# Performance work log

Hardware: AMD Instinct MI355X
Metric: run time of the kernel (lower is better)

The kernel has to match this reference:

```python
import jax, jax.numpy as jnp
import numpy as np

D_NODE, C, N_HEAD = 256, 32, 8
N_SEQ, N_RES = 256, 256
LN_EPS = 1e-5
MASK_BIAS = 1e9


def setup_inputs() -> dict:
    key = jax.random.key(0)
    ks = jax.random.split(key, 4)
    return {
        "M_raw": jax.random.normal(ks[0], (N_SEQ, N_RES, D_NODE), dtype=jnp.float32),
        "M_mask": jnp.ones((N_SEQ, N_RES), dtype=jnp.float32),
        "ln_w": jnp.ones((D_NODE,), jnp.float32),
        "ln_b": jnp.zeros((D_NODE,), jnp.float32),
        "qkv_w": jax.random.normal(ks[1], (D_NODE, 3 * N_HEAD * C), jnp.float32) * (D_NODE ** -0.5),
        "gate_w": jax.random.normal(ks[2], (D_NODE, N_HEAD * C), jnp.float32) * (D_NODE ** -0.5),
        "gate_b": jnp.ones((N_HEAD * C,), jnp.float32),
        "out_w": jax.random.normal(ks[3], (N_HEAD * C, D_NODE), jnp.float32) * ((N_HEAD * C) ** -0.5),
        "out_b": jnp.zeros((D_NODE,), jnp.float32),
    }


def reference(M_raw, M_mask, ln_w, ln_b, qkv_w, gate_w, gate_b, out_w, out_b):
    # Transpose to column-attention layout: [N_res, N_seq, d]
    M = jnp.swapaxes(M_raw, -2, -3)
    mask = jnp.swapaxes(M_mask, -1, -2)  # [N_res, N_seq]

    # LayerNorm over feature dim
    mu = jnp.mean(M, axis=-1, keepdims=True)
    var = jnp.mean(jnp.square(M - mu), axis=-1, keepdims=True)
    Mn = (M - mu) * jax.lax.rsqrt(var + LN_EPS) * ln_w + ln_b

    # QKV projection (no bias), split heads
    r, s = Mn.shape[0], Mn.shape[1]
    qkv = (Mn @ qkv_w).reshape(r, s, 3, N_HEAD, C)
    q, k, v = qkv[:, :, 0], qkv[:, :, 1], qkv[:, :, 2]  # [r, s, h, c]
    q = q * (C ** -0.5)

    # Masked attention over the sequence (column) axis
    logits = jnp.einsum('rqhc,rkhc->rhqk', q, k)
    logits = logits + (MASK_BIAS * (mask - 1.0))[:, None, None, :]
    weights = jax.nn.softmax(logits, axis=-1)
    o = jnp.einsum('rhqk,rkhc->rqhc', weights, v).reshape(r, s, N_HEAD * C)

    # Sigmoid gating and output projection
    gate = jax.nn.sigmoid(Mn @ gate_w + gate_b)
    out = (o * gate) @ out_w + out_b

    # Residual in original layout
    return M_raw + jnp.swapaxes(out, -2, -3)
```

## Files before the change

### kernel.cpp

```cpp
#include <hip/hip_runtime.h>


typedef short bf16x8 __attribute__((ext_vector_type(8)));
typedef float f32x4  __attribute__((ext_vector_type(4)));
typedef float f32x16 __attribute__((ext_vector_type(16)));

union U8 { uint w[4]; bf16x8 v; ushort u[8]; };

__device__ __forceinline__ ushort f2bf(float f) {
  uint u = __float_as_uint(f);
  u = (u + 0x7fffu + ((u >> 16) & 1u)) >> 16;
  return (ushort)u;
}

__device__ __forceinline__ uint pk2(float lo, float hi) {
  return (uint)f2bf(lo) | ((uint)f2bf(hi) << 16);
}

__device__ __forceinline__ f32x16 MFMA32(bf16x8 a, bf16x8 b, f32x16 c) {
  return __builtin_amdgcn_mfma_f32_32x32x16_bf16(a, b, c, 0, 0, 0);
}
__device__ __forceinline__ f32x4 MFMA16(bf16x8 a, bf16x8 b, f32x4 c) {
  return __builtin_amdgcn_mfma_f32_16x16x32_bf16(a, b, c, 0, 0, 0);
}

__device__ __forceinline__ bf16x8 ldG8(const ushort* __restrict__ p, int row, int ko) {
  return *(const bf16x8*)(p + (size_t)row * 256 + ko);
}

__device__ __forceinline__ f32x16 zero16() {
  f32x16 z;
  #pragma unroll
  for (int i = 0; i < 16; ++i) z[i] = 0.f;
  return z;
}

__global__ __launch_bounds__(256) void k_prep(const float* __restrict__ qkv_w,
                                              const float* __restrict__ gate_w,
                                              const float* __restrict__ out_w,
                                              ushort* __restrict__ ws) {
  __shared__ ushort t[64][72];
  const int b = blockIdx.x;
  const float* src; ushort* dst; int C, r0, c0; bool scale_q = false;
  if (b < 48)      { src = qkv_w;  dst = ws;          C = 768; r0 = (b/12)*64;      c0 = (b%12)*64; scale_q = true; }
  else if (b < 64) { int bb = b-48; src = gate_w; dst = ws + 196608; C = 256; r0 = (bb>>2)*64; c0 = (bb&3)*64; }
  else             { int bb = b-64; src = out_w;  dst = ws + 262144; C = 256; r0 = (bb>>2)*64; c0 = (bb&3)*64; }
  const int tid = threadIdx.x;
  const int cc = tid & 63, rb = tid >> 6;
  #pragma unroll
  for (int j = 0; j < 16; ++j) {
    const int rr = j*4 + rb;
    float v = src[(size_t)(r0+rr)*C + c0 + cc];
    if (scale_q && (c0+cc) < 256) v *= 0.17677669529663687f;
    t[cc][rr] = f2bf(v);
  }
  __syncthreads();
  const int dd = (tid & 31)*2, cb = tid >> 5;
  #pragma unroll
  for (int j = 0; j < 8; ++j) {
    const int c2 = j*8 + cb;
    const uint wv = (uint)t[c2][dd] | ((uint)t[c2][dd+1] << 16);
    *(uint*)(dst + (size_t)(c0+c2)*256 + r0 + dd) = wv;
  }
}

#define KOFF 0
#define VOFF 20480
#define GOFF 37376

__global__ __launch_bounds__(512, 2) void k_attn(
    const float* __restrict__ M_raw, const float* __restrict__ M_mask,
    const float* __restrict__ ln_w, const float* __restrict__ ln_b,
    const ushort* __restrict__ qkv_wT, const ushort* __restrict__ gate_wT,
    const float* __restrict__ gate_b, ushort* __restrict__ og)
{
  extern __shared__ char smem[];
  const int r    = blockIdx.x;
  const int tid  = threadIdx.x;
  const int w    = tid >> 6;
  const int lane = tid & 63;
  const int l31  = lane & 31;
  const int hl   = lane >> 5;
  const int Q0   = w << 5;
  const int s    = Q0 + l31;

  const float* rowp = M_raw + (size_t)s * 65536 + (size_t)r * 256;
  float4 xa[16], xb[16];
  float sum = 0.f, sq = 0.f;
  #pragma unroll
  for (int dt = 0; dt < 16; ++dt) {
    xa[dt] = *(const float4*)(rowp + dt*16 + hl*8);
    xb[dt] = *(const float4*)(rowp + dt*16 + hl*8 + 4);
    sum += xa[dt].x + xa[dt].y + xa[dt].z + xa[dt].w
         + xb[dt].x + xb[dt].y + xb[dt].z + xb[dt].w;
    sq  += xa[dt].x*xa[dt].x + xa[dt].y*xa[dt].y + xa[dt].z*xa[dt].z + xa[dt].w*xa[dt].w
         + xb[dt].x*xb[dt].x + xb[dt].y*xb[dt].y + xb[dt].z*xb[dt].z + xb[dt].w*xb[dt].w;
  }
  sum += __shfl_xor(sum, 32, 64);
  sq  += __shfl_xor(sq,  32, 64);
  const float mu = sum * 0.00390625f;
  const float rs = rsqrtf(sq * 0.00390625f - mu*mu + 1e-5f);
  bf16x8 mn[16];
  #pragma unroll
  for (int dt = 0; dt < 16; ++dt) {
    const float4 wa = *(const float4*)(ln_w + dt*16 + hl*8);
    const float4 wb = *(const float4*)(ln_w + dt*16 + hl*8 + 4);
    const float4 ba = *(const float4*)(ln_b + dt*16 + hl*8);
    const float4 bb = *(const float4*)(ln_b + dt*16 + hl*8 + 4);
    U8 u;
    u.w[0] = pk2((xa[dt].x-mu)*rs*wa.x+ba.x, (xa[dt].y-mu)*rs*wa.y+ba.y);
    u.w[1] = pk2((xa[dt].z-mu)*rs*wa.z+ba.z, (xa[dt].w-mu)*rs*wa.w+ba.w);
    u.w[2] = pk2((xb[dt].x-mu)*rs*wb.x+bb.x, (xb[dt].y-mu)*rs*wb.y+bb.y);
    u.w[3] = pk2((xb[dt].z-mu)*rs*wb.z+bb.z, (xb[dt].w-mu)*rs*wb.w+bb.w);
    mn[dt] = u.v;
  }

  uint m0=0, m1=0, m2=0, m3=0;
  for (int b = 0; b < 32; ++b) {
    const int k0 = ((b>>4)<<5) + (b&3) + (((b>>2)&3)<<3) + hl*4;
    m0 |= (M_mask[(size_t)(k0      )*256 + r] > 0.5f ? 1u:0u) << b;
    m1 |= (M_mask[(size_t)(k0 +  64)*256 + r] > 0.5f ? 1u:0u) << b;
    m2 |= (M_mask[(size_t)(k0 + 128)*256 + r] > 0.5f ? 1u:0u) << b;
    m3 |= (M_mask[(size_t)(k0 + 192)*256 + r] > 0.5f ? 1u:0u) << b;
  }
  const bool full = ((m0 & m1 & m2 & m3) == 0xFFFFFFFFu);

  auto mergeOp = [&](float q0, float q1, float q2, float q3,
                     float q4, float q5, float q6, float q7) -> bf16x8 {
    const uint x0 = pk2(q0, q1), x1 = pk2(q2, q3);
    const uint z0 = pk2(q4, q5), z1 = pk2(q6, q7);
    const uint xx0 = __shfl_xor(x0, 32, 64), xx1 = __shfl_xor(x1, 32, 64);
    const uint zz0 = __shfl_xor(z0, 32, 64), zz1 = __shfl_xor(z1, 32, 64);
    U8 u;
    u.w[0] = hl ? zz0 : x0;
    u.w[1] = hl ? zz1 : x1;
    u.w[2] = hl ? z0  : xx0;
    u.w[3] = hl ? z1  : xx1;
    return u.v;
  };

  auto projT = [&](const ushort* __restrict__ W, int rowbase) -> f32x16 {
    f32x16 acc = zero16();
    #pragma unroll
    for (int dt = 0; dt < 16; ++dt)
      acc = MFMA32(ldG8(W, rowbase + l31, dt*16 + hl*8), mn[dt], acc);
    return acc;
  };
  auto projN = [&](const ushort* __restrict__ W, int rowbase) -> f32x16 {
    f32x16 acc = zero16();
    #pragma unroll
    for (int dt = 0; dt < 16; ++dt)
      acc = MFMA32(mn[dt], ldG8(W, rowbase + l31, dt*16 + hl*8), acc);
    return acc;
  };
  auto packB = [&](const f32x16& q, bf16x8& lo, bf16x8& hi2) {
    lo  = mergeOp(q[0], q[1], q[2],  q[3],  q[4],  q[5],  q[6],  q[7]);
    hi2 = mergeOp(q[8], q[9], q[10], q[11], q[12], q[13], q[14], q[15]);
  };
  auto stageKV = [&](const f32x16& KA, const f32x16& VA) {
    #pragma unroll
    for (int rq = 0; rq < 4; ++rq) {
      uint2 p2;
      p2.x = pk2(KA[4*rq],   KA[4*rq+1]);
      p2.y = pk2(KA[4*rq+2], KA[4*rq+3]);
      *(uint2*)(smem + KOFF + s*80 + rq*16 + hl*8) = p2;
      p2.x = pk2(VA[4*rq],   VA[4*rq+1]);
      p2.y = pk2(VA[4*rq+2], VA[4*rq+3]);
      *(uint2*)(smem + VOFF + l31*528 + Q0*2 + rq*16 + hl*8) = p2;
    }
  };

  bf16x8 bq0, bq1;
  {
    f32x16 KA = projT(qkv_wT, 256 + 0);
    f32x16 VA = projN(qkv_wT, 512 + 0);
    stageKV(KA, VA);
    f32x16 QA = projT(qkv_wT, 0);
    packB(QA, bq0, bq1);
  }
  __syncthreads();

  for (int hd = 0; hd < 8; ++hd) {
    const int hs = hd << 5;

    float m_ = -3.0e38f, l_ = 0.f;
    f32x16 O = zero16();
    #pragma unroll
    for (int kt = 0; kt < 8; ++kt) {
      const bf16x8 a0 = *(const bf16x8*)(smem + KOFF + (kt*32 + l31)*80 + hl*16);
      const bf16x8 a1 = *(const bf16x8*)(smem + KOFF + (kt*32 + l31)*80 + 32 + hl*16);
      f32x16 S = MFMA32(a0, bq0, zero16());
      S = MFMA32(a1, bq1, S);

      float pmax = S[0];
      #pragma unroll
      for (int i = 1; i < 16; ++i) pmax = fmaxf(pmax, S[i]);
      pmax = fmaxf(pmax, __shfl_xor(pmax, 32, 64));

      if (!__all(pmax <= m_ + 8.0f)) {
        const float mnew = fmaxf(m_, pmax);
        const float sc = __expf(m_ - mnew);
        #pragma unroll
        for (int i = 0; i < 16; ++i) O[i] *= sc;
        l_ *= sc;
        m_ = mnew;
      }

      #pragma unroll
      for (int i = 0; i < 16; ++i) {
        float p = __expf(S[i] - m_);
        if (!full) {
          const int bi = kt*16 + i;
          const uint mw = (bi < 32) ? m0 : (bi < 64) ? m1 : (bi < 96) ? m2 : m3;
          p = ((mw >> (bi & 31)) & 1u) ? p : 0.f;
        }
        S[i] = p; l_ += p;
      }

      const bf16x8 pa0 = mergeOp(S[0], S[1], S[2],  S[3],  S[4],  S[5],  S[6],  S[7]);
      const bf16x8 vb0 = *(const bf16x8*)(smem + VOFF + l31*528 + kt*64 + hl*16);
      O = MFMA32(vb0, pa0, O);
      const bf16x8 pa1 = mergeOp(S[8], S[9], S[10], S[11], S[12], S[13], S[14], S[15]);
      const bf16x8 vb1 = *(const bf16x8*)(smem + VOFF + l31*528 + kt*64 + 32 + hl*16);
      O = MFMA32(vb1, pa1, O);
    }
    l_ += __shfl_xor(l_, 32, 64);
    const float inv = 1.0f / l_;

    f32x16 G = projT(gate_wT, hs);
    const int sxor = (s >> 1) & 15;
    #pragma unroll
    for (int ep = 0; ep < 8; ++ep) {
      const int e0 = 2*ep;
      const int c0 = (e0 & 3) + 8*(e0 >> 2) + 4*hl;
      const float g0 = gate_b[hs + c0];
      const float g1 = gate_b[hs + c0 + 1];
      const float v0 = O[e0]   * inv / (1.f + __expf(-(G[e0]   + g0)));
      const float v1 = O[e0+1] * inv / (1.f + __expf(-(G[e0+1] + g1)));
      const int cpair = (ep & 1) + 4*(ep >> 1) + 2*hl;
      *(uint*)(smem + GOFF + s*64 + ((cpair ^ sxor) << 2)) = pk2(v0, v1);
    }

    __syncthreads();

    uint* ogw = (uint*)og;
    const size_t ob = (size_t)(r*8 + hd) * 4096;
    #pragma unroll
    for (int j = 0; j < 8; ++j) {
      const int lin  = j*512 + tid;
      const int srow = lin >> 4;
      const int cu   = lin & 15;
      const uint wv = *(const uint*)(smem + GOFF + srow*64 + ((cu ^ ((srow >> 1) & 15)) << 2));
      ogw[ob + (size_t)srow*16 + cu] = wv;
    }

    if (hd < 7) {
      f32x16 KA = projT(qkv_wT, 256 + hs + 32);
      f32x16 VA = projN(qkv_wT, 512 + hs + 32);
      stageKV(KA, VA);
      f32x16 QA = projT(qkv_wT, hs + 32);
      packB(QA, bq0, bq1);
      __syncthreads();
    }
  }
}

__global__ __launch_bounds__(256) void k_out(
    const ushort* __restrict__ og, const ushort* __restrict__ out_wT,
    const float* __restrict__ out_b, const float* __restrict__ M_raw,
    float* __restrict__ out)
{
  const int blk  = blockIdx.x;
  const int tid  = threadIdx.x;
  const int w    = tid >> 6;
  const int lane = tid & 63;
  const int l15  = lane & 15;
  const int g    = lane >> 4;
  const int row0 = blk * 64 + w * 16;
  const int r    = row0 >> 8;
  const int s0   = row0 & 255;

  const f32x4 Z = {0.f, 0.f, 0.f, 0.f};
  f32x4 acc[16];
  #pragma unroll
  for (int nt = 0; nt < 16; ++nt) acc[nt] = Z;

  #pragma unroll
  for (int kk = 0; kk < 8; ++kk) {
    const bf16x8 a = *(const bf16x8*)(og + ((size_t)(r*8 + kk)*256 + s0 + l15)*32 + g*8);
    #pragma unroll
    for (int nt = 0; nt < 16; ++nt) {
      const bf16x8 b = ldG8(out_wT, nt*16 + l15, kk*32 + g*8);
      acc[nt] = MFMA16(a, b, acc[nt]);
    }
  }

  #pragma unroll
  for (int nt = 0; nt < 16; ++nt) {
    const int d = nt*16 + l15;
    const float ob = out_b[d];
    #pragma unroll
    for (int i = 0; i < 4; ++i) {
      const int ss = s0 + 4*g + i;
      const size_t idx = (size_t)ss * 65536 + (size_t)r * 256 + d;
      out[idx] = M_raw[idx] + acc[nt][i] + ob;
    }
  }
}

extern "C" void kernel_launch(void* const* d_in, const int* in_sizes, int n_in,
                              void* d_out, int out_size, void* d_ws, size_t ws_size,
                              hipStream_t stream) {
  const float* M_raw  = (const float*)d_in[0];
  const float* M_mask = (const float*)d_in[1];
  const float* ln_w   = (const float*)d_in[2];
  const float* ln_b   = (const float*)d_in[3];
  const float* qkv_w  = (const float*)d_in[4];
  const float* gate_w = (const float*)d_in[5];
  const float* gate_b = (const float*)d_in[6];
  const float* out_w  = (const float*)d_in[7];
  const float* out_b  = (const float*)d_in[8];

  ushort* ws      = (ushort*)d_ws;
  ushort* qkv_wT  = ws;
  ushort* gate_wT = ws + 196608;
  ushort* out_wT  = ws + 262144;
  ushort* og      = ws + 327680;

  hipFuncSetAttribute(reinterpret_cast<const void*>(k_attn),
                      hipFuncAttributeMaxDynamicSharedMemorySize, 53760);

  hipLaunchKernelGGL(k_prep, dim3(80), dim3(256), 0, stream, qkv_w, gate_w, out_w, ws);
  hipLaunchKernelGGL(k_attn, dim3(256), dim3(512), 53760, stream,
                     M_raw, M_mask, ln_w, ln_b, qkv_wT, gate_wT, gate_b, og);
  hipLaunchKernelGGL(k_out, dim3(1024), dim3(256), 0, stream,
                     og, out_wT, out_b, M_raw, (float*)d_out);
}
```

Before: 386.9 us.

## Split attention heads across two blocks per residue and break MFMA dependency chains

Launches the attention kernel with a second grid dimension so each block handles four heads instead of eight, doubling the block count from 256 to 512 to fill more CUs. Each block now redoes the LayerNorm and the load of its residue column, duplicating that global read. Projection and PV accumulations are split into two independent MFMA accumulators, and the row max uses a tree reduction, to shorten serial dependency chains at the cost of extra registers.

```diff
diff --git a/kernel.cpp b/kernel.cpp
--- a/kernel.cpp
+++ b/kernel.cpp
@@ -76,6 +76,7 @@
 {
   extern __shared__ char smem[];
   const int r    = blockIdx.x;
+  const int hg   = blockIdx.y;
   const int tid  = threadIdx.x;
   const int w    = tid >> 6;
   const int lane = tid & 63;
@@ -140,18 +141,22 @@
   };
 
   auto projT = [&](const ushort* __restrict__ W, int rowbase) -> f32x16 {
-    f32x16 acc = zero16();
-    #pragma unroll
-    for (int dt = 0; dt < 16; ++dt)
-      acc = MFMA32(ldG8(W, rowbase + l31, dt*16 + hl*8), mn[dt], acc);
-    return acc;
+    f32x16 a0 = zero16(), a1 = zero16();
+    #pragma unroll
+    for (int dt = 0; dt < 8; ++dt) {
+      a0 = MFMA32(ldG8(W, rowbase + l31, dt*16 + hl*8),       mn[dt],   a0);
+      a1 = MFMA32(ldG8(W, rowbase + l31, (dt+8)*16 + hl*8),   mn[dt+8], a1);
+    }
+    return a0 + a1;
   };
   auto projN = [&](const ushort* __restrict__ W, int rowbase) -> f32x16 {
-    f32x16 acc = zero16();
-    #pragma unroll
-    for (int dt = 0; dt < 16; ++dt)
-      acc = MFMA32(mn[dt], ldG8(W, rowbase + l31, dt*16 + hl*8), acc);
-    return acc;
+    f32x16 a0 = zero16(), a1 = zero16();
+    #pragma unroll
+    for (int dt = 0; dt < 8; ++dt) {
+      a0 = MFMA32(mn[dt],   ldG8(W, rowbase + l31, dt*16 + hl*8),     a0);
+      a1 = MFMA32(mn[dt+8], ldG8(W, rowbase + l31, (dt+8)*16 + hl*8), a1);
+    }
+    return a0 + a1;
   };
   auto packB = [&](const f32x16& q, bf16x8& lo, bf16x8& hi2) {
     lo  = mergeOp(q[0], q[1], q[2],  q[3],  q[4],  q[5],  q[6],  q[7]);
@@ -170,21 +175,23 @@
     }
   };
 
+  const int h0 = hg * 4;
   bf16x8 bq0, bq1;
   {
-    f32x16 KA = projT(qkv_wT, 256 + 0);
-    f32x16 VA = projN(qkv_wT, 512 + 0);
+    f32x16 KA = projT(qkv_wT, 256 + h0*32);
+    f32x16 VA = projN(qkv_wT, 512 + h0*32);
     stageKV(KA, VA);
-    f32x16 QA = projT(qkv_wT, 0);
+    f32x16 QA = projT(qkv_wT, h0*32);
     packB(QA, bq0, bq1);
   }
   __syncthreads();
 
-  for (int hd = 0; hd < 8; ++hd) {
+  for (int hh = 0; hh < 4; ++hh) {
+    const int hd = h0 + hh;
     const int hs = hd << 5;
 
     float m_ = -3.0e38f, l_ = 0.f;
-    f32x16 O = zero16();
+    f32x16 Oa = zero16(), Ob = zero16();
     #pragma unroll
     for (int kt = 0; kt < 8; ++kt) {
       const bf16x8 a0 = *(const bf16x8*)(smem + KOFF + (kt*32 + l31)*80 + hl*16);
@@ -192,16 +199,20 @@
       f32x16 S = MFMA32(a0, bq0, zero16());
       S = MFMA32(a1, bq1, S);
 
-      float pmax = S[0];
-      #pragma unroll
-      for (int i = 1; i < 16; ++i) pmax = fmaxf(pmax, S[i]);
+      float b0 = fmaxf(S[0],S[1]),  b1 = fmaxf(S[2],S[3]);
+      float b2 = fmaxf(S[4],S[5]),  b3 = fmaxf(S[6],S[7]);
+      float b4 = fmaxf(S[8],S[9]),  b5 = fmaxf(S[10],S[11]);
+      float b6 = fmaxf(S[12],S[13]),b7 = fmaxf(S[14],S[15]);
+      b0 = fmaxf(b0,b1); b2 = fmaxf(b2,b3); b4 = fmaxf(b4,b5); b6 = fmaxf(b6,b7);
+      b0 = fmaxf(b0,b2); b4 = fmaxf(b4,b6);
+      float pmax = fmaxf(b0,b4);
       pmax = fmaxf(pmax, __shfl_xor(pmax, 32, 64));
 
       if (!__all(pmax <= m_ + 8.0f)) {
         const float mnew = fmaxf(m_, pmax);
         const float sc = __expf(m_ - mnew);
         #pragma unroll
-        for (int i = 0; i < 16; ++i) O[i] *= sc;
+        for (int i = 0; i < 16; ++i) { Oa[i] *= sc; Ob[i] *= sc; }
         l_ *= sc;
         m_ = mnew;
       }
@@ -219,13 +230,14 @@
 
       const bf16x8 pa0 = mergeOp(S[0], S[1], S[2],  S[3],  S[4],  S[5],  S[6],  S[7]);
       const bf16x8 vb0 = *(const bf16x8*)(smem + VOFF + l31*528 + kt*64 + hl*16);
-      O = MFMA32(vb0, pa0, O);
+      Oa = MFMA32(vb0, pa0, Oa);
       const bf16x8 pa1 = mergeOp(S[8], S[9], S[10], S[11], S[12], S[13], S[14], S[15]);
       const bf16x8 vb1 = *(const bf16x8*)(smem + VOFF + l31*528 + kt*64 + 32 + hl*16);
-      O = MFMA32(vb1, pa1, O);
+      Ob = MFMA32(vb1, pa1, Ob);
     }
     l_ += __shfl_xor(l_, 32, 64);
     const float inv = 1.0f / l_;
+    const f32x16 O = Oa + Ob;
 
     f32x16 G = projT(gate_wT, hs);
     const int sxor = (s >> 1) & 15;
@@ -254,7 +266,7 @@
       ogw[ob + (size_t)srow*16 + cu] = wv;
     }
 
-    if (hd < 7) {
+    if (hh < 3) {
       f32x16 KA = projT(qkv_wT, 256 + hs + 32);
       f32x16 VA = projN(qkv_wT, 512 + hs + 32);
       stageKV(KA, VA);
@@ -331,7 +343,7 @@
                       hipFuncAttributeMaxDynamicSharedMemorySize, 53760);
 
   hipLaunchKernelGGL(k_prep, dim3(80), dim3(256), 0, stream, qkv_w, gate_w, out_w, ws);
-  hipLaunchKernelGGL(k_attn, dim3(256), dim3(512), 53760, stream,
+  hipLaunchKernelGGL(k_attn, dim3(256, 2), dim3(512), 53760, stream,
                      M_raw, M_mask, ln_w, ln_b, qkv_wT, gate_wT, gate_b, og);
   hipLaunchKernelGGL(k_out, dim3(1024), dim3(256), 0, stream,
                      og, out_wT, out_b, M_raw, (float*)d_out);
```

New measurement: 431.4 us. 1.12x slower.
